# Performance work log

Measured on AMD Instinct MI355X. Metric: run time of the kernel, lower is better.

Reference implementation:

```python
import jax, jax.numpy as jnp
import numpy as np

B, S, D, H = 2, 2048, 1024, 16
HEAD_DIM = D // H  # 64


def setup_inputs() -> dict:
    key = jax.random.key(0)
    ks = jax.random.split(key, 7)
    x = jax.random.normal(ks[0], (B, S, D), dtype=jnp.float32)
    W_q = jax.random.normal(ks[1], (D, D), dtype=jnp.float32) * 0.02
    W_k = jax.random.normal(ks[2], (D, D), dtype=jnp.float32) * 0.02
    W_v = jax.random.normal(ks[3], (D, D), dtype=jnp.float32) * 0.02
    W_o = jax.random.normal(ks[4], (D, D), dtype=jnp.float32) * 0.02 / np.sqrt(2 * 12)
    b_o = jnp.zeros((D,), dtype=jnp.float32)
    # Ragged prefix attention_mask: per-row valid lengths in [S/2, S];
    # row 0 forced to full length so max_valid_len == S statically (jit-safe).
    lengths = jax.random.randint(ks[5], (B,), S // 2, S + 1)
    lengths = lengths.at[0].set(S)
    attention_mask = (jnp.arange(S)[None, :] < lengths[:, None]).astype(jnp.float32)
    return {"x": x, "attention_mask": attention_mask, "W_q": W_q, "W_k": W_k,
            "W_v": W_v, "W_o": W_o, "b_o": b_o}


def reference(x, attention_mask, W_q, W_k, W_v, W_o, b_o):
    b, s, d = x.shape
    h, hd = H, HEAD_DIM
    # QKV projections (no bias, qkv_bias=False)
    q = (x @ W_q.T).reshape(b, s, h, hd).transpose(0, 2, 1, 3)  # [b,h,s,hd]
    # Masking keys/values at invalid (padded) positions; for prefix masks this
    # is exactly the module's per-batch packing loop (max_valid_len == s).
    m = attention_mask[:, None, :, None]  # [b,1,s,1]
    k = ((x @ W_k.T).reshape(b, s, h, hd).transpose(0, 2, 1, 3)) * m
    v = ((x @ W_v.T).reshape(b, s, h, hd).transpose(0, 2, 1, 3)) * m
    # Naive causal attention, same op order as the torch module:
    # mask with -inf first, then scale by 1/sqrt(head_dim), then softmax.
    causal = jnp.triu(jnp.ones((s, s), dtype=bool), 1)  # True above diagonal
    scores = jnp.einsum('bhqd,bhkd->bhqk', q, k)
    scores = jnp.where(causal[None, None], -jnp.inf, scores)
    att = jax.nn.softmax(scores / jnp.sqrt(jnp.float32(hd)), axis=-1)
    ctx = jnp.einsum('bhqk,bhkd->bhqd', att, v)  # [b,h,s,hd]
    ctx = ctx.transpose(0, 2, 1, 3).reshape(b, s, d)
    # Output projection (dropout is inference no-op)
    return ctx @ W_o.T + b_o
```

## Files before the change

### kernel.cpp

```cpp
#include <hip/hip_runtime.h>

#define B_  2
#define S_  2048
#define D_  1024
#define H_  16
#define HD_ 64
#define N3_ 3072
#define M_  4096

typedef _Float16 f16;
typedef _Float16 f16x2 __attribute__((ext_vector_type(2)));
typedef _Float16 f16x4 __attribute__((ext_vector_type(4)));
typedef _Float16 f16x8 __attribute__((ext_vector_type(8)));
typedef float    f32x4 __attribute__((ext_vector_type(4)));

__device__ __forceinline__ void async16(const f16* g, f16* l) {
  __builtin_amdgcn_global_load_lds(
      (const __attribute__((address_space(1))) unsigned int*)g,
      (__attribute__((address_space(3))) unsigned int*)l, 16, 0, 0);
}

__global__ __launch_bounds__(256)
void cvt_f32_f16(const float* __restrict__ src, f16* __restrict__ dst,
                 int n4, float scale) {
  int i = blockIdx.x * 256 + threadIdx.x;
  if (i >= n4) return;
  float4 v = ((const float4*)src)[i];
  f16x4 o = { (f16)(v.x * scale), (f16)(v.y * scale),
              (f16)(v.z * scale), (f16)(v.w * scale) };
  ((f16x4*)dst)[i] = o;
}

__global__ __launch_bounds__(256)
void cvt_weights(const float* __restrict__ Wq, const float* __restrict__ Wk,
                 const float* __restrict__ Wv, const float* __restrict__ Wo,
                 f16* __restrict__ dst, float qscale) {
  const int m = blockIdx.y;
  const float* src = (m == 0) ? Wq : (m == 1) ? Wk : (m == 2) ? Wv : Wo;
  const float scale = (m == 0) ? qscale : 1.0f;
  int i = blockIdx.x * 256 + threadIdx.x;
  float4 v = ((const float4*)src)[i];
  f16x4 o = { (f16)(v.x * scale), (f16)(v.y * scale),
              (f16)(v.z * scale), (f16)(v.w * scale) };
  ((f16x4*)(dst + (size_t)m * D_ * D_))[i] = o;
}

template<int QKV>
__global__ __launch_bounds__(256)
void gemm_nt(const f16* __restrict__ A, const f16* __restrict__ Bw,
             f16* __restrict__ Cq, float* __restrict__ Cf,
             f16* __restrict__ vtout,
             const float* __restrict__ mask, const float* __restrict__ bias,
             int Ndim, int Kdim) {
  __shared__ f16 As[128 * 64];
  __shared__ f16 Bs[128 * 64];

  const int tid  = threadIdx.x;
  const int lane = tid & 63;
  const int w    = tid >> 6;
  const int lcol = lane & 15;
  const int quad = lane >> 4;
  const int lx   = lcol & 7;
  const int wave_m = w >> 1, wave_n = w & 1;

  const int m0 = blockIdx.y * 128;
  const int n0 = blockIdx.x * 128;

  const int rr  = lane >> 3;
  const int gch = (lane & 7) ^ rr;

  const f16* gA[4];
  const f16* gB[4];
  f16* lA[4];
  f16* lB[4];
#pragma unroll
  for (int i = 0; i < 4; i++) {
    int seg = i * 4 + w;
    int row = seg * 8 + rr;
    gA[i] = A  + (size_t)(m0 + row) * Kdim + gch * 8;
    gB[i] = Bw + (size_t)(n0 + row) * Kdim + gch * 8;
    lA[i] = As + seg * 512;
    lB[i] = Bs + seg * 512;
  }

  int offA[4], offB[4];
#pragma unroll
  for (int i = 0; i < 4; i++) {
    offA[i] = (wave_m * 64 + i * 16 + lcol) * 64;
    offB[i] = (wave_n * 64 + i * 16 + lcol) * 64;
  }

  const f32x4 zero = {0.f, 0.f, 0.f, 0.f};
  f32x4 acc[4][4];
#pragma unroll
  for (int i = 0; i < 4; i++)
#pragma unroll
    for (int j = 0; j < 4; j++) acc[i][j] = zero;

  for (int k0 = 0; k0 < Kdim; k0 += 64) {
    __syncthreads();
#pragma unroll
    for (int i = 0; i < 4; i++) async16(gA[i] + k0, lA[i]);
#pragma unroll
    for (int i = 0; i < 4; i++) async16(gB[i] + k0, lB[i]);
    __syncthreads();

#pragma unroll
    for (int ks = 0; ks < 2; ks++) {
      const int co = ((quad + 4 * ks) ^ lx) * 8;
      f16x8 af[4], bf[4];
#pragma unroll
      for (int i = 0; i < 4; i++) af[i] = *(const f16x8*)(As + offA[i] + co);
#pragma unroll
      for (int i = 0; i < 4; i++) bf[i] = *(const f16x8*)(Bs + offB[i] + co);
#pragma unroll
      for (int mi = 0; mi < 4; mi++)
#pragma unroll
        for (int ni = 0; ni < 4; ni++)
          acc[mi][ni] = __builtin_amdgcn_mfma_f32_16x16x32_f16(
              af[mi], bf[ni], acc[mi][ni], 0, 0, 0);
    }
  }

  if (QKV && n0 >= 2 * D_) {
#pragma unroll
    for (int mi = 0; mi < 4; mi++) {
      const int mgb = m0 + wave_m * 64 + mi * 16 + quad * 4;
      const int b = mgb >> 11, s = mgb & (S_ - 1);
      const float mk0 = mask[mgb], mk1 = mask[mgb + 1];
      const float mk2 = mask[mgb + 2], mk3 = mask[mgb + 3];
#pragma unroll
      for (int ni = 0; ni < 4; ni++) {
        const int vcol = n0 - 2 * D_ + wave_n * 64 + ni * 16 + lcol;
        f16x4 v = { (f16)(acc[mi][ni][0] * mk0), (f16)(acc[mi][ni][1] * mk1),
                    (f16)(acc[mi][ni][2] * mk2), (f16)(acc[mi][ni][3] * mk3) };
        *(f16x4*)(vtout +
                  ((size_t)(b * 16 + (vcol >> 6)) * 64 + (vcol & 63)) * S_ + s) = v;
      }
    }
  } else {
    const bool kmask = QKV && (n0 >= D_);
#pragma unroll
    for (int mi = 0; mi < 4; mi++) {
#pragma unroll
      for (int r = 0; r < 4; r++) {
        int mg = m0 + wave_m * 64 + mi * 16 + quad * 4 + r;
        float mk = kmask ? mask[mg] : 1.0f;
#pragma unroll
        for (int ni = 0; ni < 4; ni++) {
          int ng = n0 + wave_n * 64 + ni * 16 + lcol;
          float v = acc[mi][ni][r] * mk;
          if (QKV) Cq[(size_t)mg * Ndim + ng] = (f16)v;
          else     Cf[(size_t)mg * Ndim + ng] = v + bias[ng];
        }
      }
    }
  }
}

__global__ __launch_bounds__(256)
void flash_attn4(const f16* __restrict__ qkv, const f16* __restrict__ vt,
                 f16* __restrict__ ctx) {
  __shared__ f16 Ks[64 * 64];
  __shared__ f16 Vs[64 * 64];

  const int tid  = threadIdx.x;
  const int lane = tid & 63;
  const int w    = tid >> 6;
  const int lcol = lane & 15;
  const int quad = lane >> 4;
  const int lx   = lcol & 7;

  const int id   = blockIdx.x;
  const int bh   = (id & 7) + 8 * ((id >> 3) & 3);
  const int pair = id >> 5;
  const int b    = bh >> 4, h = bh & 15;
  const int qtA  = 31 - pair;
  const int qtB  = pair;

  const int rsub = lane >> 3;
  const int gch  = (lane & 7) ^ rsub;
  const int krow0 = w * 8 + rsub;
  const int krow1 = 32 + w * 8 + rsub;
  const f16* Kg = qkv + (size_t)b * S_ * N3_ + D_ + h * HD_;
  const f16* Vg = vt + (size_t)bh * HD_ * S_;
  f16* ldsK0 = Ks + (w * 8) * 64;
  f16* ldsK1 = Ks + (32 + w * 8) * 64;
  f16* ldsV0 = Vs + (w * 8) * 64;
  f16* ldsV1 = Vs + (32 + w * 8) * 64;

  const f32x4 zero = {0.f, 0.f, 0.f, 0.f};

  const int qrowA = qtA * 64 + w * 16 + lcol;
  const int qrowB = qtB * 64 + w * 16 + lcol;
  const f16* QpA = qkv + (size_t)(b * S_ + qrowA) * N3_ + h * HD_;
  const f16* QpB = qkv + (size_t)(b * S_ + qrowB) * N3_ + h * HD_;
  const f16x8 qbA0 = *(const f16x8*)(QpA + quad * 8);
  const f16x8 qbA1 = *(const f16x8*)(QpA + 32 + quad * 8);
  const f16x8 qbB0 = *(const f16x8*)(QpB + quad * 8);
  const f16x8 qbB1 = *(const f16x8*)(QpB + 32 + quad * 8);

  f32x4 oA[4], oB[4];
  float lpA = 0.f, lpB = 0.f;
#pragma unroll
  for (int i = 0; i < 4; i++) { oA[i] = zero; oB[i] = zero; }

  auto mask_diag = [&](f32x4* sc) {
#pragma unroll
    for (int ct = 0; ct < 4; ct++) {
      int koff = ct * 16 + quad * 4;
      int qoff = w * 16 + lcol;
#pragma unroll
      for (int r = 0; r < 4; r++)
        if (koff + r > qoff) sc[ct][r] = -1e30f;
    }
  };
  auto softmax_tiles = [&](f32x4* sc, f16x4* pf, float& lp) {
#pragma unroll
    for (int ct = 0; ct < 4; ct++) {
      float e0 = exp2f(sc[ct][0]);
      float e1 = exp2f(sc[ct][1]);
      float e2 = exp2f(sc[ct][2]);
      float e3 = exp2f(sc[ct][3]);
      lp += (e0 + e1) + (e2 + e3);
      f16x2 lo = __builtin_bit_cast(f16x2, __builtin_amdgcn_cvt_pkrtz(e0, e1));
      f16x2 hi = __builtin_bit_cast(f16x2, __builtin_amdgcn_cvt_pkrtz(e2, e3));
      f16x4 p = { lo[0], lo[1], hi[0], hi[1] };
      pf[ct] = p;
    }
  };

  for (int kt = 0; kt <= qtA; kt++) {
    const int kbase = kt * 64;
    __syncthreads();
    async16(Kg + (size_t)(kbase + krow0) * N3_ + gch * 8, ldsK0);
    async16(Kg + (size_t)(kbase + krow1) * N3_ + gch * 8, ldsK1);
    async16(Vg + (size_t)krow0 * S_ + kbase + gch * 8, ldsV0);
    async16(Vg + (size_t)krow1 * S_ + kbase + gch * 8, ldsV1);
    __syncthreads();

    const bool doB = (kt <= qtB);

    f16x8 kf0[4], kf1[4];
    f32x4 scA[4], scB[4];
#pragma unroll
    for (int ct = 0; ct < 4; ct++) {
      const f16* kr = Ks + (ct * 16 + lcol) * 64;
      kf0[ct] = *(const f16x8*)(kr + ((quad    ) ^ lx) * 8);
      kf1[ct] = *(const f16x8*)(kr + ((quad + 4) ^ lx) * 8);
      f32x4 z = zero;
      z = __builtin_amdgcn_mfma_f32_16x16x32_f16(kf0[ct], qbA0, z, 0, 0, 0);
      z = __builtin_amdgcn_mfma_f32_16x16x32_f16(kf1[ct], qbA1, z, 0, 0, 0);
      scA[ct] = z;
    }
    if (doB) {
#pragma unroll
      for (int ct = 0; ct < 4; ct++) {
        f32x4 z = zero;
        z = __builtin_amdgcn_mfma_f32_16x16x32_f16(kf0[ct], qbB0, z, 0, 0, 0);
        z = __builtin_amdgcn_mfma_f32_16x16x32_f16(kf1[ct], qbB1, z, 0, 0, 0);
        scB[ct] = z;
      }
    }

    if (kt == qtA) mask_diag(scA);
    if (doB && kt == qtB) mask_diag(scB);

    f16x4 pfA[4], pfB[4];
    softmax_tiles(scA, pfA, lpA);
    if (doB) softmax_tiles(scB, pfB, lpB);

#pragma unroll
    for (int ht = 0; ht < 4; ht++) {
      const f16* vr = Vs + (ht * 16 + lcol) * 64 + (quad & 1) * 4;
      f16x4 vf[4];
#pragma unroll
      for (int ct = 0; ct < 4; ct++)
        vf[ct] = *(const f16x4*)(vr + (((2 * ct + (quad >> 1)) ^ lx) * 8));
#pragma unroll
      for (int ct = 0; ct < 4; ct++)
        oA[ht] = __builtin_amdgcn_mfma_f32_16x16x16f16(vf[ct], pfA[ct], oA[ht], 0, 0, 0);
      if (doB) {
#pragma unroll
        for (int ct = 0; ct < 4; ct++)
          oB[ht] = __builtin_amdgcn_mfma_f32_16x16x16f16(vf[ct], pfB[ct], oB[ht], 0, 0, 0);
      }
    }
  }

  lpA += __shfl_xor(lpA, 16);
  lpA += __shfl_xor(lpA, 32);
  lpB += __shfl_xor(lpB, 16);
  lpB += __shfl_xor(lpB, 32);
  const float invA = 1.f / lpA;
  const float invB = 1.f / lpB;
  f16* cpA = ctx + (size_t)(b * S_ + qrowA) * D_ + h * HD_ + quad * 4;
  f16* cpB = ctx + (size_t)(b * S_ + qrowB) * D_ + h * HD_ + quad * 4;
#pragma unroll
  for (int ht = 0; ht < 4; ht++) {
    f16x4 ovA = { (f16)(oA[ht][0] * invA), (f16)(oA[ht][1] * invA),
                  (f16)(oA[ht][2] * invA), (f16)(oA[ht][3] * invA) };
    *(f16x4*)(cpA + ht * 16) = ovA;
    f16x4 ovB = { (f16)(oB[ht][0] * invB), (f16)(oB[ht][1] * invB),
                  (f16)(oB[ht][2] * invB), (f16)(oB[ht][3] * invB) };
    *(f16x4*)(cpB + ht * 16) = ovB;
  }
}

extern "C" void kernel_launch(void* const* d_in, const int* in_sizes, int n_in,
                              void* d_out, int out_size, void* d_ws, size_t ws_size,
                              hipStream_t stream) {
  (void)in_sizes; (void)n_in; (void)out_size; (void)ws_size;
  const float* x  = (const float*)d_in[0];
  const float* am = (const float*)d_in[1];
  const float* Wq = (const float*)d_in[2];
  const float* Wk = (const float*)d_in[3];
  const float* Wv = (const float*)d_in[4];
  const float* Wo = (const float*)d_in[5];
  const float* bo = (const float*)d_in[6];
  float* out = (float*)d_out;

  f16* ws   = (f16*)d_ws;
  f16* wqkv = ws;
  f16* wo16 = wqkv + (size_t)3 * D_ * D_;
  f16* xb   = wo16 + (size_t)D_ * D_;
  f16* qkvb = xb + (size_t)M_ * D_;
  f16* vtb  = qkvb + (size_t)M_ * N3_;
  f16* ctxb = vtb + (size_t)M_ * D_;

  const float qscale = 0.125f * 1.4426950408889634f;

  cvt_f32_f16<<<dim3(M_ * D_ / 1024), 256, 0, stream>>>(x, xb, M_ * D_ / 4, 1.0f);
  cvt_weights<<<dim3(D_ * D_ / 1024, 4), 256, 0, stream>>>(Wq, Wk, Wv, Wo, wqkv, qscale);

  gemm_nt<1><<<dim3(N3_ / 128, M_ / 128), 256, 0, stream>>>(
      xb, wqkv, qkvb, nullptr, vtb, am, nullptr, N3_, D_);
  flash_attn4<<<dim3(512), 256, 0, stream>>>(qkvb, vtb, ctxb);
  gemm_nt<0><<<dim3(D_ / 128, M_ / 128), 256, 0, stream>>>(
      ctxb, wo16, nullptr, out, nullptr, nullptr, bo, D_, D_);
}
```

Before: 199.9 us.

## Fuse x fp32-to-fp16 conversion into QKV GEMM with register-staged prefetch

Removes the separate kernel that converts x to fp16. The QKV GEMM now reads fp32 x directly and converts it in registers before storing to LDS. Both GEMMs replace async global-to-LDS loads with register-staged loads, prefetching the next K tile while the current one is computed. This drops one launch and a write plus re-read of the fp16 x buffer, at the cost of reading twice as many A bytes in the GEMM and using more registers for staging.

Result: faster. 193.5 us (-3.2%).

```diff
diff --git a/kernel.cpp b/kernel.cpp
--- a/kernel.cpp
+++ b/kernel.cpp
@@ -20,15 +20,8 @@
       (__attribute__((address_space(3))) unsigned int*)l, 16, 0, 0);
 }
 
-__global__ __launch_bounds__(256)
-void cvt_f32_f16(const float* __restrict__ src, f16* __restrict__ dst,
-                 int n4, float scale) {
-  int i = blockIdx.x * 256 + threadIdx.x;
-  if (i >= n4) return;
-  float4 v = ((const float4*)src)[i];
-  f16x4 o = { (f16)(v.x * scale), (f16)(v.y * scale),
-              (f16)(v.z * scale), (f16)(v.w * scale) };
-  ((f16x4*)dst)[i] = o;
+__device__ __forceinline__ f16x2 pkrtz(float a, float b) {
+  return __builtin_bit_cast(f16x2, __builtin_amdgcn_cvt_pkrtz(a, b));
 }
 
 __global__ __launch_bounds__(256)
@@ -45,9 +38,10 @@
   ((f16x4*)(dst + (size_t)m * D_ * D_))[i] = o;
 }
 
-template<int QKV>
+template<int QKV, bool AF32>
 __global__ __launch_bounds__(256)
-void gemm_nt(const f16* __restrict__ A, const f16* __restrict__ Bw,
+void gemm_nt(const float* __restrict__ A32, const f16* __restrict__ A16,
+             const f16* __restrict__ Bw,
              f16* __restrict__ Cq, float* __restrict__ Cf,
              f16* __restrict__ vtout,
              const float* __restrict__ mask, const float* __restrict__ bias,
@@ -67,20 +61,19 @@
   const int n0 = blockIdx.x * 128;
 
   const int rr  = lane >> 3;
-  const int gch = (lane & 7) ^ rr;
-
-  const f16* gA[4];
-  const f16* gB[4];
+  const int pch = lane & 7;
+  const int gch = pch ^ rr;
+
+  int rowg[4];
   f16* lA[4];
   f16* lB[4];
 #pragma unroll
   for (int i = 0; i < 4; i++) {
     int seg = i * 4 + w;
     int row = seg * 8 + rr;
-    gA[i] = A  + (size_t)(m0 + row) * Kdim + gch * 8;
-    gB[i] = Bw + (size_t)(n0 + row) * Kdim + gch * 8;
-    lA[i] = As + seg * 512;
-    lB[i] = Bs + seg * 512;
+    rowg[i] = row;
+    lA[i] = As + row * 64 + pch * 8;
+    lB[i] = Bs + row * 64 + pch * 8;
   }
 
   int offA[4], offB[4];
@@ -97,13 +90,46 @@
 #pragma unroll
     for (int j = 0; j < 4; j++) acc[i][j] = zero;
 
+  float4 ra0[4], ra1[4];
+  f16x8  ra16[4];
+  f16x8  rb[4];
+
+  auto load_tile = [&](int k0) {
+#pragma unroll
+    for (int i = 0; i < 4; i++) {
+      if (AF32) {
+        const float* p = A32 + (size_t)(m0 + rowg[i]) * Kdim + k0 + gch * 8;
+        ra0[i] = *(const float4*)p;
+        ra1[i] = *(const float4*)(p + 4);
+      } else {
+        ra16[i] = *(const f16x8*)(A16 + (size_t)(m0 + rowg[i]) * Kdim + k0 + gch * 8);
+      }
+      rb[i] = *(const f16x8*)(Bw + (size_t)(n0 + rowg[i]) * Kdim + k0 + gch * 8);
+    }
+  };
+  auto write_tile = [&]() {
+#pragma unroll
+    for (int i = 0; i < 4; i++) {
+      if (AF32) {
+        f16x2 c0 = pkrtz(ra0[i].x, ra0[i].y);
+        f16x2 c1 = pkrtz(ra0[i].z, ra0[i].w);
+        f16x2 c2 = pkrtz(ra1[i].x, ra1[i].y);
+        f16x2 c3 = pkrtz(ra1[i].z, ra1[i].w);
+        f16x8 v = { c0[0], c0[1], c1[0], c1[1], c2[0], c2[1], c3[0], c3[1] };
+        *(f16x8*)lA[i] = v;
+      } else {
+        *(f16x8*)lA[i] = ra16[i];
+      }
+      *(f16x8*)lB[i] = rb[i];
+    }
+  };
+
+  load_tile(0);
   for (int k0 = 0; k0 < Kdim; k0 += 64) {
     __syncthreads();
-#pragma unroll
-    for (int i = 0; i < 4; i++) async16(gA[i] + k0, lA[i]);
-#pragma unroll
-    for (int i = 0; i < 4; i++) async16(gB[i] + k0, lB[i]);
+    write_tile();
     __syncthreads();
+    if (k0 + 64 < Kdim) load_tile(k0 + 64);
 
 #pragma unroll
     for (int ks = 0; ks < 2; ks++) {
@@ -223,8 +249,8 @@
       float e2 = exp2f(sc[ct][2]);
       float e3 = exp2f(sc[ct][3]);
       lp += (e0 + e1) + (e2 + e3);
-      f16x2 lo = __builtin_bit_cast(f16x2, __builtin_amdgcn_cvt_pkrtz(e0, e1));
-      f16x2 hi = __builtin_bit_cast(f16x2, __builtin_amdgcn_cvt_pkrtz(e2, e3));
+      f16x2 lo = pkrtz(e0, e1);
+      f16x2 hi = pkrtz(e2, e3);
       f16x4 p = { lo[0], lo[1], hi[0], hi[1] };
       pf[ct] = p;
     }
@@ -323,19 +349,17 @@
   f16* ws   = (f16*)d_ws;
   f16* wqkv = ws;
   f16* wo16 = wqkv + (size_t)3 * D_ * D_;
-  f16* xb   = wo16 + (size_t)D_ * D_;
-  f16* qkvb = xb + (size_t)M_ * D_;
+  f16* qkvb = wo16 + (size_t)D_ * D_;
   f16* vtb  = qkvb + (size_t)M_ * N3_;
   f16* ctxb = vtb + (size_t)M_ * D_;
 
   const float qscale = 0.125f * 1.4426950408889634f;
 
-  cvt_f32_f16<<<dim3(M_ * D_ / 1024), 256, 0, stream>>>(x, xb, M_ * D_ / 4, 1.0f);
   cvt_weights<<<dim3(D_ * D_ / 1024, 4), 256, 0, stream>>>(Wq, Wk, Wv, Wo, wqkv, qscale);
 
-  gemm_nt<1><<<dim3(N3_ / 128, M_ / 128), 256, 0, stream>>>(
-      xb, wqkv, qkvb, nullptr, vtb, am, nullptr, N3_, D_);
+  gemm_nt<1, true><<<dim3(N3_ / 128, M_ / 128), 256, 0, stream>>>(
+      x, nullptr, wqkv, qkvb, nullptr, vtb, am, nullptr, N3_, D_);
   flash_attn4<<<dim3(512), 256, 0, stream>>>(qkvb, vtb, ctxb);
-  gemm_nt<0><<<dim3(D_ / 128, M_ / 128), 256, 0, stream>>>(
-      ctxb, wo16, nullptr, out, nullptr, nullptr, bo, D_, D_);
-}
+  gemm_nt<0, false><<<dim3(D_ / 128, M_ / 128), 256, 0, stream>>>(
+      nullptr, ctxb, wo16, nullptr, out, nullptr, nullptr, bo, D_, D_);
+}
```

## Double-buffer LDS tiles in GEMM and flash attention to overlap loads

Applied to the files above, without the earlier changes.

Both the GEMM and the attention kernel now keep two LDS buffers. Each iteration issues the async global-to-LDS copy for the next tile before computing on the current one, which removes one barrier per iteration and is meant to hide global load latency behind MFMA work. In exchange, the GEMM's LDS footprint doubles to 64KB per block, which can lower occupancy. The overlap only materialises if the compiler does not place a full vmcnt wait before the LDS reads.

Measured after the change: 196.3 us. About the same (-1.8%).

```diff
diff --git a/kernel.cpp b/kernel.cpp
--- a/kernel.cpp
+++ b/kernel.cpp
@@ -18,6 +18,10 @@
   __builtin_amdgcn_global_load_lds(
       (const __attribute__((address_space(1))) unsigned int*)g,
       (__attribute__((address_space(3))) unsigned int*)l, 16, 0, 0);
+}
+
+__device__ __forceinline__ f16x2 pkrtz(float a, float b) {
+  return __builtin_bit_cast(f16x2, __builtin_amdgcn_cvt_pkrtz(a, b));
 }
 
 __global__ __launch_bounds__(256)
@@ -52,8 +56,8 @@
              f16* __restrict__ vtout,
              const float* __restrict__ mask, const float* __restrict__ bias,
              int Ndim, int Kdim) {
-  __shared__ f16 As[128 * 64];
-  __shared__ f16 Bs[128 * 64];
+  __shared__ f16 As[2][128 * 64];
+  __shared__ f16 Bs[2][128 * 64];
 
   const int tid  = threadIdx.x;
   const int lane = tid & 63;
@@ -71,17 +75,22 @@
 
   const f16* gA[4];
   const f16* gB[4];
-  f16* lA[4];
-  f16* lB[4];
+  int soff[4];
 #pragma unroll
   for (int i = 0; i < 4; i++) {
     int seg = i * 4 + w;
     int row = seg * 8 + rr;
     gA[i] = A  + (size_t)(m0 + row) * Kdim + gch * 8;
     gB[i] = Bw + (size_t)(n0 + row) * Kdim + gch * 8;
-    lA[i] = As + seg * 512;
-    lB[i] = Bs + seg * 512;
-  }
+    soff[i] = seg * 512;
+  }
+
+  auto stage = [&](int k0, int buf) {
+#pragma unroll
+    for (int i = 0; i < 4; i++) async16(gA[i] + k0, As[buf] + soff[i]);
+#pragma unroll
+    for (int i = 0; i < 4; i++) async16(gB[i] + k0, Bs[buf] + soff[i]);
+  };
 
   int offA[4], offB[4];
 #pragma unroll
@@ -97,22 +106,22 @@
 #pragma unroll
     for (int j = 0; j < 4; j++) acc[i][j] = zero;
 
-  for (int k0 = 0; k0 < Kdim; k0 += 64) {
+  const int niter = Kdim >> 6;
+  stage(0, 0);
+  for (int it = 0; it < niter; it++) {
     __syncthreads();
-#pragma unroll
-    for (int i = 0; i < 4; i++) async16(gA[i] + k0, lA[i]);
-#pragma unroll
-    for (int i = 0; i < 4; i++) async16(gB[i] + k0, lB[i]);
-    __syncthreads();
-
+    if (it + 1 < niter) stage((it + 1) << 6, (it + 1) & 1);
+
+    const f16* Ab = As[it & 1];
+    const f16* Bb = Bs[it & 1];
 #pragma unroll
     for (int ks = 0; ks < 2; ks++) {
       const int co = ((quad + 4 * ks) ^ lx) * 8;
       f16x8 af[4], bf[4];
 #pragma unroll
-      for (int i = 0; i < 4; i++) af[i] = *(const f16x8*)(As + offA[i] + co);
-#pragma unroll
-      for (int i = 0; i < 4; i++) bf[i] = *(const f16x8*)(Bs + offB[i] + co);
+      for (int i = 0; i < 4; i++) af[i] = *(const f16x8*)(Ab + offA[i] + co);
+#pragma unroll
+      for (int i = 0; i < 4; i++) bf[i] = *(const f16x8*)(Bb + offB[i] + co);
 #pragma unroll
       for (int mi = 0; mi < 4; mi++)
 #pragma unroll
@@ -159,10 +168,10 @@
 }
 
 __global__ __launch_bounds__(256)
-void flash_attn4(const f16* __restrict__ qkv, const f16* __restrict__ vt,
+void flash_attn5(const f16* __restrict__ qkv, const f16* __restrict__ vt,
                  f16* __restrict__ ctx) {
-  __shared__ f16 Ks[64 * 64];
-  __shared__ f16 Vs[64 * 64];
+  __shared__ f16 Ks[2][64 * 64];
+  __shared__ f16 Vs[2][64 * 64];
 
   const int tid  = threadIdx.x;
   const int lane = tid & 63;
@@ -180,14 +189,20 @@
 
   const int rsub = lane >> 3;
   const int gch  = (lane & 7) ^ rsub;
+  const int ko0  = (w * 8) * 64;
+  const int ko1  = (32 + w * 8) * 64;
   const int krow0 = w * 8 + rsub;
   const int krow1 = 32 + w * 8 + rsub;
   const f16* Kg = qkv + (size_t)b * S_ * N3_ + D_ + h * HD_;
   const f16* Vg = vt + (size_t)bh * HD_ * S_;
-  f16* ldsK0 = Ks + (w * 8) * 64;
-  f16* ldsK1 = Ks + (32 + w * 8) * 64;
-  f16* ldsV0 = Vs + (w * 8) * 64;
-  f16* ldsV1 = Vs + (32 + w * 8) * 64;
+
+  auto stage = [&](int kt, int buf) {
+    const int kbase = kt * 64;
+    async16(Kg + (size_t)(kbase + krow0) * N3_ + gch * 8, Ks[buf] + ko0);
+    async16(Kg + (size_t)(kbase + krow1) * N3_ + gch * 8, Ks[buf] + ko1);
+    async16(Vg + (size_t)krow0 * S_ + kbase + gch * 8, Vs[buf] + ko0);
+    async16(Vg + (size_t)krow1 * S_ + kbase + gch * 8, Vs[buf] + ko1);
+  };
 
   const f32x4 zero = {0.f, 0.f, 0.f, 0.f};
 
@@ -223,29 +238,27 @@
       float e2 = exp2f(sc[ct][2]);
       float e3 = exp2f(sc[ct][3]);
       lp += (e0 + e1) + (e2 + e3);
-      f16x2 lo = __builtin_bit_cast(f16x2, __builtin_amdgcn_cvt_pkrtz(e0, e1));
-      f16x2 hi = __builtin_bit_cast(f16x2, __builtin_amdgcn_cvt_pkrtz(e2, e3));
+      f16x2 lo = pkrtz(e0, e1);
+      f16x2 hi = pkrtz(e2, e3);
       f16x4 p = { lo[0], lo[1], hi[0], hi[1] };
       pf[ct] = p;
     }
   };
 
+  stage(0, 0);
   for (int kt = 0; kt <= qtA; kt++) {
-    const int kbase = kt * 64;
     __syncthreads();
-    async16(Kg + (size_t)(kbase + krow0) * N3_ + gch * 8, ldsK0);
-    async16(Kg + (size_t)(kbase + krow1) * N3_ + gch * 8, ldsK1);
-    async16(Vg + (size_t)krow0 * S_ + kbase + gch * 8, ldsV0);
-    async16(Vg + (size_t)krow1 * S_ + kbase + gch * 8, ldsV1);
-    __syncthreads();
-
+    if (kt + 1 <= qtA) stage(kt + 1, (kt + 1) & 1);
+
+    const f16* Kb = Ks[kt & 1];
+    const f16* Vb = Vs[kt & 1];
     const bool doB = (kt <= qtB);
 
     f16x8 kf0[4], kf1[4];
     f32x4 scA[4], scB[4];
 #pragma unroll
     for (int ct = 0; ct < 4; ct++) {
-      const f16* kr = Ks + (ct * 16 + lcol) * 64;
+      const f16* kr = Kb + (ct * 16 + lcol) * 64;
       kf0[ct] = *(const f16x8*)(kr + ((quad    ) ^ lx) * 8);
       kf1[ct] = *(const f16x8*)(kr + ((quad + 4) ^ lx) * 8);
       f32x4 z = zero;
@@ -272,7 +285,7 @@
 
 #pragma unroll
     for (int ht = 0; ht < 4; ht++) {
-      const f16* vr = Vs + (ht * 16 + lcol) * 64 + (quad & 1) * 4;
+      const f16* vr = Vb + (ht * 16 + lcol) * 64 + (quad & 1) * 4;
       f16x4 vf[4];
 #pragma unroll
       for (int ct = 0; ct < 4; ct++)
@@ -335,7 +348,7 @@
 
   gemm_nt<1><<<dim3(N3_ / 128, M_ / 128), 256, 0, stream>>>(
       xb, wqkv, qkvb, nullptr, vtb, am, nullptr, N3_, D_);
-  flash_attn4<<<dim3(512), 256, 0, stream>>>(qkvb, vtb, ctxb);
+  flash_attn5<<<dim3(512), 256, 0, stream>>>(qkvb, vtb, ctxb);
   gemm_nt<0><<<dim3(D_ / 128, M_ / 128), 256, 0, stream>>>(
       ctxb, wo16, nullptr, out, nullptr, nullptr, bo, D_, D_);
 }
```
